# Kernel optimization log

Hardware: AMD Instinct MI355X
Metric: run time of the kernel (lower is better)

The kernel has to match this reference:

```python
import math
import jax, jax.numpy as jnp
import numpy as np

PATCH_NUMS = (1, 2, 3, 4, 5, 6, 8, 10, 13, 16)
_lens = [p * p for p in PATCH_NUMS]
_cum = np.concatenate([[0], np.cumsum(_lens)])
BEGIN_ENDS = [(int(_cum[i]), int(_cum[i + 1])) for i in range(len(PATCH_NUMS))]
L_TOTAL = int(_cum[-1])  # 680

B, C = 32, 1024
S, P, M, R, NCAT = 10, 8, 4, 8, 22
SLOTS = P * M  # 32 slots per scale
MEM_RANK = 64
ALPHA_HID = 128


def setup_inputs() -> dict:
    key = jax.random.key(0)
    ks = jax.random.split(key, 24)
    inp = {}
    inp['x'] = jax.random.normal(ks[0], (B, L_TOTAL, C), jnp.float32)
    # -1 means CFG-unconditional sample (no category memory)
    inp['category_ids'] = jax.random.randint(ks[1], (B,), -1, NCAT)
    # shared memory, orthogonal-ish init rescaled to xavier std sqrt(2/(C+C))
    inp['shared_memory'] = jax.random.normal(ks[2], (S, SLOTS, C)) * math.sqrt(1.0 / C)
    inp['cat_A'] = jax.random.normal(ks[3], (NCAT, S, R)) * 0.01
    inp['cat_B'] = jax.random.normal(ks[4], (S, R, SLOTS * C)) * (1.0 / math.sqrt(R))
    inp['cat_emb'] = jax.random.normal(ks[5], (NCAT, C)) * 0.02
    inp['scale_emb'] = jax.random.normal(ks[6], (S, C)) * 0.02
    inp['Wq'] = jax.random.normal(ks[7], (C, C)) * (1.0 / math.sqrt(C))
    inp['Wk'] = jax.random.normal(ks[8], (C, C)) * (1.0 / math.sqrt(C))
    inp['Wv'] = jax.random.normal(ks[9], (C, C)) * (1.0 / math.sqrt(C))
    inp['aW1'] = jax.random.normal(ks[10], (3 * C, ALPHA_HID)) * (1.0 / math.sqrt(3 * C))
    inp['ab1'] = jnp.zeros((ALPHA_HID,), jnp.float32)
    inp['aW2'] = jax.random.normal(ks[11], (ALPHA_HID, 1)) * 0.01  # init zeros in torch; small random to exercise math
    inp['ab2'] = jnp.full((1,), -1.0, jnp.float32)
    inp['kW1'] = jax.random.normal(ks[12], (C, MEM_RANK)) * (1.0 / math.sqrt(C))
    inp['kb1'] = jnp.zeros((MEM_RANK,), jnp.float32)
    inp['kW2'] = jax.random.normal(ks[13], (MEM_RANK, C)) * (1.0 / math.sqrt(MEM_RANK))
    inp['kb2'] = jnp.zeros((C,), jnp.float32)
    inp['vW1'] = jax.random.normal(ks[14], (C, MEM_RANK)) * (1.0 / math.sqrt(C))
    inp['vb1'] = jnp.zeros((MEM_RANK,), jnp.float32)
    inp['vW2'] = jax.random.normal(ks[15], (MEM_RANK, C)) * (1.0 / math.sqrt(MEM_RANK))
    inp['vb2'] = jnp.zeros((C,), jnp.float32)
    inp['gk_logit'] = jnp.float32(-2.0)  # block_idx=0, depth=16
    inp['gv_logit'] = jnp.float32(-2.0)
    inp['log_temp'] = jnp.float32(math.log(0.1))
    return inp


def reference(x, category_ids, shared_memory, cat_A, cat_B, cat_emb, scale_emb,
              Wq, Wk, Wv, aW1, ab1, aW2, ab2,
              kW1, kb1, kW2, kb2, vW1, vb1, vW2, vb2,
              gk_logit, gv_logit, log_temp):
    Bb, L, Cc = x.shape
    temp = jnp.clip(jnp.exp(log_temp), 0.05, 1.0)
    inv_sqrt_c = 1.0 / math.sqrt(Cc)

    query = x @ Wq                              # [B, L, C]
    shared_k = shared_memory @ Wk               # [S, slots, C]
    shared_v = shared_memory @ Wv

    valid = (category_ids >= 0)                 # [B]
    cid = jnp.clip(category_ids, 0, None)
    a_all = cat_A[cid]                          # [B, S, R]
    ce = cat_emb[cid]                           # [B, C]

    outs = []
    for i, (s, e) in enumerate(BEGIN_ENDS):
        q = query[:, s:e, :]                    # [B, Ls, C]
        Ls = e - s
        V = i + 1                               # visible scales
        # --- shared retrieval over visible slots ---
        ks_ = shared_k[:V].reshape(V * SLOTS, Cc)
        vs_ = shared_v[:V].reshape(V * SLOTS, Cc)
        attn_s = jax.nn.softmax((q @ ks_.T) * inv_sqrt_c / temp, axis=-1)
        o_s = attn_s @ vs_                      # [B, Ls, C]
        # --- per-category memory: shared + low-rank residual ---
        delta = jnp.einsum('bvr,vrd->bvd', a_all[:, :V], cat_B[:V])
        delta = delta.reshape(Bb, V, SLOTS, Cc)
        cat_mem = (shared_memory[:V][None] + delta).reshape(Bb, V * SLOTS, Cc)
        kc = cat_mem @ Wk                       # [B, Vs, C]
        vc = cat_mem @ Wv
        attn_c = jax.nn.softmax(jnp.einsum('bld,bsd->bls', q, kc) * inv_sqrt_c / temp, axis=-1)
        o_c = jnp.einsum('bls,bsd->bld', attn_c, vc)
        # --- learned alpha blend (zeroed for invalid / CFG categories) ---
        ai = jnp.concatenate([
            q,
            jnp.broadcast_to(ce[:, None, :], (Bb, Ls, Cc)),
            jnp.broadcast_to(scale_emb[i][None, None, :], (Bb, Ls, Cc)),
        ], axis=-1)                             # [B, Ls, 3C]
        h = jax.nn.gelu(ai @ aW1 + ab1, approximate=False)
        alpha = jax.nn.sigmoid(h @ aW2 + ab2)   # [B, Ls, 1]
        alpha = jnp.where(valid[:, None, None], alpha, 0.0)
        outs.append(o_s + alpha * (o_c - o_s))

    mem = jnp.concatenate(outs, axis=1)         # [B, L, C]
    mem_k = jax.nn.sigmoid(gk_logit) * ((mem @ kW1 + kb1) @ kW2 + kb2)
    mem_v = jax.nn.sigmoid(gv_logit) * ((mem @ vW1 + vb1) @ vW2 + vb2)
    zero = jnp.float32(0.0)
    return mem_k, mem_v, zero, zero
```

## Files before the change

kernel.cpp:

```cpp
#include <hip/hip_runtime.h>
#include <math.h>

#define NB 32
#define NC 1024
#define LTOT 680

typedef unsigned short u16;
typedef __bf16 bf16x8 __attribute__((ext_vector_type(8)));
typedef float floatx4 __attribute__((ext_vector_type(4)));

__device__ __forceinline__ u16 f2bf(float f)
{
    union { float f; unsigned u; } v; v.f = f;
    unsigned u = v.u;
    u += 0x7FFFu + ((u >> 16) & 1u);
    return (u16)(u >> 16);
}

__device__ __forceinline__ float bf2f(unsigned u)
{
    union { unsigned u; float f; } v; v.u = u << 16; return v.f;
}

__device__ __forceinline__ void gload16(const u16* g, u16* l)
{
    typedef __attribute__((address_space(1))) const void gv_t;
    typedef __attribute__((address_space(3))) void lv_t;
    __builtin_amdgcn_global_load_lds(
        (gv_t*)(unsigned long long)(const void*)g,
        (lv_t*)(unsigned int)(unsigned long long)(void*)l,
        16, 0, 0);
}

__device__ __forceinline__ void slot_decode(int s, int* prow, int* pcq)
{
    *prow = ((s >> 7) << 4) | (s & 15);
    *pcq  = (((s >> 6) & 1) << 2) | ((s >> 4) & 3);
}

template<int AFP32, int OUTBF>
__global__ __launch_bounds__(256) void gemm_mfma(
    const void* __restrict__ Av, const u16* __restrict__ BT,
    float* __restrict__ C, int M, int N, int K, int lda,
    const float* __restrict__ bias, const float* __restrict__ scale_logit)
{
    __shared__ __align__(16) u16 As[16 * 64 * 8];
    __shared__ __align__(16) u16 Bs[16 * 64 * 8];

    const int tid  = threadIdx.x;
    const int m0   = blockIdx.y << 7;
    const int n0   = blockIdx.x << 7;
    const int wave = tid >> 6;
    const int lane = tid & 63;
    const int mh   = wave & 1;
    const int nh   = wave >> 1;

    const u16* aSrc[4];
    const u16* bSrc[4];
#pragma unroll
    for (int p = 0; p < 4; ++p) {
        int s, row, cq;
        s = tid + (p << 8);
        slot_decode(s, &row, &cq);
        if (!AFP32) {
            int gr = m0 + row; if (gr > M - 1) gr = M - 1;
            aSrc[p] = (const u16*)Av + (size_t)gr * lda + (cq << 3);
        }
        int gn = n0 + row; if (gn > N - 1) gn = N - 1;
        bSrc[p] = BT + (size_t)gn * K + (cq << 3);
    }

    floatx4 acc[4][4];
#pragma unroll
    for (int i = 0; i < 4; ++i)
#pragma unroll
        for (int j = 0; j < 4; ++j) acc[i][j] = (floatx4){0.f, 0.f, 0.f, 0.f};

    for (int k0 = 0; k0 < K; k0 += 64) {
        __syncthreads();
        if (AFP32) {
            const float* A = (const float*)Av;
#pragma unroll
            for (int p = 0; p < 8; ++p) {
                int q   = tid + (p << 8);
                int row = q >> 4;
                int fq  = q & 15;
                int gr  = m0 + row; if (gr > M - 1) gr = M - 1;
                const float4 a4 = *(const float4*)(A + (size_t)gr * lda + k0 + (fq << 2));
                int kh = fq >> 3, quad = (fq >> 1) & 3, jh = fq & 1;
                u16* d = &As[((((row >> 4) << 1) | kh) * 64 + (quad << 4) + (row & 15)) * 8 + (jh << 2)];
                d[0] = f2bf(a4.x); d[1] = f2bf(a4.y); d[2] = f2bf(a4.z); d[3] = f2bf(a4.w);
            }
        } else {
#pragma unroll
            for (int p = 0; p < 4; ++p)
                gload16(aSrc[p] + k0, As + ((wave << 6) + (p << 8)) * 8);
        }
#pragma unroll
        for (int p = 0; p < 4; ++p)
            gload16(bSrc[p] + k0, Bs + ((wave << 6) + (p << 8)) * 8);
        __syncthreads();
#pragma unroll
        for (int kh = 0; kh < 2; ++kh) {
            bf16x8 a[4], b[4];
#pragma unroll
            for (int i = 0; i < 4; ++i)
                a[i] = *(const bf16x8*)&As[(((((mh << 2) + i) << 1) | kh) * 64 + lane) * 8];
#pragma unroll
            for (int j = 0; j < 4; ++j)
                b[j] = *(const bf16x8*)&Bs[(((((nh << 2) + j) << 1) | kh) * 64 + lane) * 8];
#pragma unroll
            for (int i = 0; i < 4; ++i)
#pragma unroll
                for (int j = 0; j < 4; ++j)
                    acc[i][j] = __builtin_amdgcn_mfma_f32_16x16x32_bf16(a[i], b[j], acc[i][j], 0, 0, 0);
        }
    }

    float scale = 1.f;
    if (scale_logit) scale = 1.f / (1.f + __expf(-scale_logit[0]));
    const int col = lane & 15, rquad = lane >> 4;
#pragma unroll
    for (int i = 0; i < 4; ++i) {
#pragma unroll
        for (int j = 0; j < 4; ++j) {
#pragma unroll
            for (int r = 0; r < 4; ++r) {
                int gr = m0 + (mh << 6) + (i << 4) + (rquad << 2) + r;
                int gc = n0 + (nh << 6) + (j << 4) + col;
                if (gr < M && gc < N) {
                    float bb = bias ? bias[gc] : 0.f;
                    float val = scale * (acc[i][j][r] + bb);
                    if (OUTBF) ((u16*)C)[(size_t)gr * N + gc] = f2bf(val);
                    else       C[(size_t)gr * N + gc] = val;
                }
            }
        }
    }
}

__global__ __launch_bounds__(256) void gemm_logits(
    const u16* __restrict__ Q, const u16* __restrict__ skb,
    const u16* __restrict__ kcb, float* __restrict__ out)
{
    __shared__ __align__(16) u16 As[16 * 64 * 8];
    __shared__ __align__(16) u16 Bs[16 * 64 * 8];

    const int tid  = threadIdx.x;
    const int m0   = blockIdx.x << 7;
    const int n0   = blockIdx.y << 7;
    const int b    = blockIdx.z;
    const int wave = tid >> 6;
    const int lane = tid & 63;
    const int mh   = wave & 1;
    const int nh   = wave >> 1;

    const u16* Ab = Q   + (size_t)b * 680 * 1024;
    const u16* KC = kcb + (size_t)b * 320 * 1024;

    const u16* aSrc[4];
    const u16* bSrc[4];
#pragma unroll
    for (int p = 0; p < 4; ++p) {
        int s, row, cq;
        s = tid + (p << 8);
        slot_decode(s, &row, &cq);
        int gr = m0 + row; if (gr > 679) gr = 679;
        aSrc[p] = Ab + (size_t)gr * 1024 + (cq << 3);
        int gn = n0 + row;
        bSrc[p] = ((gn < 320) ? (skb + (size_t)gn * 1024)
                              : (KC + (size_t)(gn - 320) * 1024)) + (cq << 3);
    }

    floatx4 acc[4][4];
#pragma unroll
    for (int i = 0; i < 4; ++i)
#pragma unroll
        for (int j = 0; j < 4; ++j) acc[i][j] = (floatx4){0.f, 0.f, 0.f, 0.f};

    for (int k0 = 0; k0 < 1024; k0 += 64) {
        __syncthreads();
#pragma unroll
        for (int p = 0; p < 4; ++p)
            gload16(aSrc[p] + k0, As + ((wave << 6) + (p << 8)) * 8);
#pragma unroll
        for (int p = 0; p < 4; ++p)
            gload16(bSrc[p] + k0, Bs + ((wave << 6) + (p << 8)) * 8);
        __syncthreads();
#pragma unroll
        for (int kh = 0; kh < 2; ++kh) {
            bf16x8 a[4], bb[4];
#pragma unroll
            for (int i = 0; i < 4; ++i)
                a[i] = *(const bf16x8*)&As[(((((mh << 2) + i) << 1) | kh) * 64 + lane) * 8];
#pragma unroll
            for (int j = 0; j < 4; ++j)
                bb[j] = *(const bf16x8*)&Bs[(((((nh << 2) + j) << 1) | kh) * 64 + lane) * 8];
#pragma unroll
            for (int i = 0; i < 4; ++i)
#pragma unroll
                for (int j = 0; j < 4; ++j)
                    acc[i][j] = __builtin_amdgcn_mfma_f32_16x16x32_bf16(a[i], bb[j], acc[i][j], 0, 0, 0);
        }
    }

    const int col = lane & 15, rquad = lane >> 4;
#pragma unroll
    for (int i = 0; i < 4; ++i)
#pragma unroll
        for (int j = 0; j < 4; ++j)
#pragma unroll
            for (int r = 0; r < 4; ++r) {
                int gr = m0 + (mh << 6) + (i << 4) + (rquad << 2) + r;
                int gc = n0 + (nh << 6) + (j << 4) + col;
                if (gr < 680)
                    out[((size_t)b * 680 + gr) * 640 + gc] = acc[i][j][r];
            }
}

__global__ __launch_bounds__(256) void gemm_pv(
    const u16* __restrict__ P, const u16* __restrict__ svT,
    const u16* __restrict__ vcT, u16* __restrict__ out)
{
    __shared__ __align__(16) u16 As[16 * 64 * 8];
    __shared__ __align__(16) u16 Bs[16 * 64 * 8];

    const int tid  = threadIdx.x;
    const int m0   = blockIdx.x << 7;
    const int n0   = blockIdx.y << 7;
    const int b    = blockIdx.z;
    const int wave = tid >> 6;
    const int lane = tid & 63;
    const int mh   = wave & 1;
    const int nh   = wave >> 1;

    const u16* aSrc[4];
    const u16* bSrcS[4];
    const u16* bSrcC[4];
#pragma unroll
    for (int p = 0; p < 4; ++p) {
        int s, row, cq;
        s = tid + (p << 8);
        slot_decode(s, &row, &cq);
        int gr = m0 + row; if (gr > 679) gr = 679;
        aSrc[p] = P + ((size_t)b * 680 + gr) * 1280 + (cq << 3);
        int gn = n0 + row;
        bSrcS[p] = svT + (size_t)gn * 320 + (cq << 3);
        bSrcC[p] = vcT + ((size_t)b * 1024 + gn) * 320 + (cq << 3);
    }

    floatx4 acc[4][4];
#pragma unroll
    for (int i = 0; i < 4; ++i)
#pragma unroll
        for (int j = 0; j < 4; ++j) acc[i][j] = (floatx4){0.f, 0.f, 0.f, 0.f};

    for (int k0 = 0; k0 < 640; k0 += 64) {
        __syncthreads();
#pragma unroll
        for (int p = 0; p < 4; ++p)
            gload16(aSrc[p] + k0, As + ((wave << 6) + (p << 8)) * 8);
#pragma unroll
        for (int p = 0; p < 4; ++p) {
            const u16* bp = (k0 < 320) ? (bSrcS[p] + k0) : (bSrcC[p] + (k0 - 320));
            gload16(bp, Bs + ((wave << 6) + (p << 8)) * 8);
        }
        __syncthreads();
#pragma unroll
        for (int kh = 0; kh < 2; ++kh) {
            bf16x8 a[4], bb[4];
#pragma unroll
            for (int i = 0; i < 4; ++i)
                a[i] = *(const bf16x8*)&As[(((((mh << 2) + i) << 1) | kh) * 64 + lane) * 8];
#pragma unroll
            for (int j = 0; j < 4; ++j)
                bb[j] = *(const bf16x8*)&Bs[(((((nh << 2) + j) << 1) | kh) * 64 + lane) * 8];
#pragma unroll
            for (int i = 0; i < 4; ++i)
#pragma unroll
                for (int j = 0; j < 4; ++j)
                    acc[i][j] = __builtin_amdgcn_mfma_f32_16x16x32_bf16(a[i], bb[j], acc[i][j], 0, 0, 0);
        }
    }

    const int col = lane & 15, rquad = lane >> 4;
#pragma unroll
    for (int i = 0; i < 4; ++i)
#pragma unroll
        for (int j = 0; j < 4; ++j)
#pragma unroll
            for (int r = 0; r < 4; ++r) {
                int gr = m0 + (mh << 6) + (i << 4) + (rquad << 2) + r;
                int gc = n0 + (nh << 6) + (j << 4) + col;
                if (gr < 680)
                    out[((size_t)b * 680 + gr) * 1024 + gc] = f2bf(acc[i][j][r]);
            }
}

__global__ __launch_bounds__(256) void gemm_halpha(
    const u16* __restrict__ Q, const u16* __restrict__ W,
    const float* __restrict__ ceW, const float* __restrict__ seW,
    const int* __restrict__ cat_ids, u16* __restrict__ h)
{
    __shared__ __align__(16) u16 As[16 * 64 * 8];
    __shared__ __align__(16) u16 Bs[16 * 64 * 8];

    const int tid  = threadIdx.x;
    const int m0   = blockIdx.x << 7;
    const int wave = tid >> 6;
    const int lane = tid & 63;
    const int mh   = wave & 1;
    const int nh   = wave >> 1;

    const u16* aSrc[4];
    const u16* bSrc[4];
#pragma unroll
    for (int p = 0; p < 4; ++p) {
        int s, row, cq;
        s = tid + (p << 8);
        slot_decode(s, &row, &cq);
        aSrc[p] = Q + (size_t)(m0 + row) * 1024 + (cq << 3);
        bSrc[p] = W + (size_t)row * 1024 + (cq << 3);
    }

    floatx4 acc[4][4];
#pragma unroll
    for (int i = 0; i < 4; ++i)
#pragma unroll
        for (int j = 0; j < 4; ++j) acc[i][j] = (floatx4){0.f, 0.f, 0.f, 0.f};

    for (int k0 = 0; k0 < 1024; k0 += 64) {
        __syncthreads();
#pragma unroll
        for (int p = 0; p < 4; ++p)
            gload16(aSrc[p] + k0, As + ((wave << 6) + (p << 8)) * 8);
#pragma unroll
        for (int p = 0; p < 4; ++p)
            gload16(bSrc[p] + k0, Bs + ((wave << 6) + (p << 8)) * 8);
        __syncthreads();
#pragma unroll
        for (int kh = 0; kh < 2; ++kh) {
            bf16x8 a[4], bb[4];
#pragma unroll
            for (int i = 0; i < 4; ++i)
                a[i] = *(const bf16x8*)&As[(((((mh << 2) + i) << 1) | kh) * 64 + lane) * 8];
#pragma unroll
            for (int j = 0; j < 4; ++j)
                bb[j] = *(const bf16x8*)&Bs[(((((nh << 2) + j) << 1) | kh) * 64 + lane) * 8];
#pragma unroll
            for (int i = 0; i < 4; ++i)
#pragma unroll
                for (int j = 0; j < 4; ++j)
                    acc[i][j] = __builtin_amdgcn_mfma_f32_16x16x32_bf16(a[i], bb[j], acc[i][j], 0, 0, 0);
        }
    }

    const int se_[9] = {1,5,14,30,55,91,155,255,424};
    const int col = lane & 15, rquad = lane >> 4;
#pragma unroll
    for (int i = 0; i < 4; ++i) {
#pragma unroll
        for (int r = 0; r < 4; ++r) {
            int gr = m0 + (mh << 6) + (i << 4) + (rquad << 2) + r;
            int b  = gr / 680;
            int l  = gr - b * 680;
            int isc = 0;
#pragma unroll
            for (int k = 0; k < 9; ++k) if (l >= se_[k]) isc = k + 1;
            int cid = cat_ids[b]; if (cid < 0) cid = 0;
            const float* cw = ceW + cid * 128;
            const float* sw = seW + isc * 128;
#pragma unroll
            for (int j = 0; j < 4; ++j) {
                int gc = (nh << 6) + (j << 4) + col;
                float val = acc[i][j][r] + cw[gc] + sw[gc];
                float g = 0.5f * val * (1.0f + erff(val * 0.70710678118654752f));
                h[(size_t)gr * 128 + gc] = f2bf(g);
            }
        }
    }
}

__global__ __launch_bounds__(256) void alpha_reduce(
    const u16* __restrict__ h, const float* __restrict__ aW2,
    const float* __restrict__ ab2, const int* __restrict__ cat_ids,
    float* __restrict__ alpha)
{
    const int wave = threadIdx.x >> 6;
    const int lane = threadIdx.x & 63;
    const int row  = (blockIdx.x << 2) + wave;

    const unsigned pk = *(const unsigned*)(h + (size_t)row * 128 + (lane << 1));
    float s = bf2f(pk) * aW2[lane << 1] + bf2f(pk >> 16) * aW2[(lane << 1) + 1];
#pragma unroll
    for (int k = 32; k >= 1; k >>= 1) s += __shfl_xor(s, k);
    if (lane == 0) {
        int b = row / 680;
        float al = 0.f;
        if (cat_ids[b] >= 0) al = 1.f / (1.f + expf(-(s + ab2[0])));
        alpha[row] = al;
    }
}

__global__ __launch_bounds__(256) void softmax_kernel(
    float* __restrict__ logits, const float* __restrict__ alpha,
    const float* __restrict__ log_temp)
{
    const int tid  = threadIdx.x;
    const int w    = tid >> 6;
    const int lane = tid & 63;
    const int b    = blockIdx.y;
    const int l    = (blockIdx.x << 2) + w;

    const int se[10] = {1,5,14,30,55,91,155,255,424,680};
    int isc = 0;
#pragma unroll
    for (int k = 0; k < 9; ++k) if (l >= se[k]) isc = k + 1;
    const int NK = (isc + 1) << 5;

    float temp = __expf(log_temp[0]);
    temp = fminf(fmaxf(temp, 0.05f), 1.0f);
    const float Ksc = 0.03125f / temp;

    float* row = logits + ((size_t)b * 680 + l) * 640;

    float ls[5], lc[5];
#pragma unroll
    for (int u = 0; u < 5; ++u) {
        int j = lane + (u << 6);
        bool v = j < NK;
        ls[u] = v ? row[j]       : -1e30f;
        lc[u] = v ? row[320 + j] : -1e30f;
    }
    float mxs = -1e30f, mxc = -1e30f;
#pragma unroll
    for (int u = 0; u < 5; ++u) { mxs = fmaxf(mxs, ls[u]); mxc = fmaxf(mxc, lc[u]); }
#pragma unroll
    for (int k = 32; k >= 1; k >>= 1) {
        mxs = fmaxf(mxs, __shfl_xor(mxs, k));
        mxc = fmaxf(mxc, __shfl_xor(mxc, k));
    }
    float es[5], ec[5], ss = 0.f, sc = 0.f;
#pragma unroll
    for (int u = 0; u < 5; ++u) {
        int j = lane + (u << 6);
        bool v = j < NK;
        es[u] = v ? __expf((ls[u] - mxs) * Ksc) : 0.f;
        ec[u] = v ? __expf((lc[u] - mxc) * Ksc) : 0.f;
        ss += es[u]; sc += ec[u];
    }
#pragma unroll
    for (int k = 32; k >= 1; k >>= 1) {
        ss += __shfl_xor(ss, k);
        sc += __shfl_xor(sc, k);
    }
    const float al = alpha[b * LTOT + l];
    const float wS = (1.f - al) / ss;
    const float wC = al / sc;

    u16* po = (u16*)row;
#pragma unroll
    for (int u = 0; u < 5; ++u) {
        int j = lane + (u << 6);
        po[j]       = f2bf(es[u] * wS);
        po[320 + j] = f2bf(ec[u] * wC);
    }
}

__global__ __launch_bounds__(256) void castbf(
    const float* __restrict__ in, u16* __restrict__ out, int n4)
{
    int i = blockIdx.x * 256 + threadIdx.x;
    const int stride = gridDim.x * 256;
    for (; i < n4; i += stride) {
        const float4 v = ((const float4*)in)[i];
        uint2 o;
        o.x = (unsigned)f2bf(v.x) | ((unsigned)f2bf(v.y) << 16);
        o.y = (unsigned)f2bf(v.z) | ((unsigned)f2bf(v.w) << 16);
        ((uint2*)out)[i] = o;
    }
}

__global__ __launch_bounds__(256) void tcast(
    const float* __restrict__ in, u16* __restrict__ out, int R, int Cc)
{
    __shared__ float t[32][33];
    const int bx = blockIdx.x * 32;
    const int by = blockIdx.y * 32;
    const int x = threadIdx.x & 31;
    const int y0 = threadIdx.x >> 5;
#pragma unroll
    for (int yy = y0; yy < 32; yy += 8)
        t[yy][x] = (by + yy < R && bx + x < Cc)
                 ? in[(size_t)(by + yy) * Cc + bx + x] : 0.f;
    __syncthreads();
#pragma unroll
    for (int yy = y0; yy < 32; yy += 8)
        if (bx + yy < Cc && by + x < R)
            out[(size_t)(bx + yy) * R + by + x] = f2bf(t[x][yy]);
}

__global__ __launch_bounds__(256) void transpose32(
    const float* __restrict__ in, float* __restrict__ out, int R, int Cc)
{
    __shared__ float t[32][33];
    const int bx = blockIdx.x * 32;
    const int by = blockIdx.y * 32;
    const int x = threadIdx.x & 31;
    const int y0 = threadIdx.x >> 5;
#pragma unroll
    for (int yy = y0; yy < 32; yy += 8)
        t[yy][x] = (by + yy < R && bx + x < Cc)
                 ? in[(size_t)(by + yy) * Cc + bx + x] : 0.f;
    __syncthreads();
#pragma unroll
    for (int yy = y0; yy < 32; yy += 8)
        if (bx + yy < Cc && by + x < R)
            out[(size_t)(bx + yy) * R + by + x] = t[x][yy];
}

__global__ __launch_bounds__(256) void build_kc(
    const float* __restrict__ sk, const float* __restrict__ catBK,
    const float* __restrict__ cat_A, const int* __restrict__ cat_ids,
    u16* __restrict__ kc)
{
    const int b = blockIdx.x;
    const int jrow = blockIdx.y;
    const int v = jrow >> 5, slot = jrow & 31;
    int cid = cat_ids[b]; if (cid < 0) cid = 0;
    float a[8];
#pragma unroll
    for (int r = 0; r < 8; ++r) a[r] = cat_A[(cid * 10 + v) * 8 + r];
    const int c = threadIdx.x << 2;
    float4 acc = *(const float4*)(sk + (size_t)jrow * 1024 + c);
#pragma unroll
    for (int r = 0; r < 8; ++r) {
        const float4 bv = *(const float4*)(catBK + (size_t)((v * 8 + r) * 32 + slot) * 1024 + c);
        acc.x = fmaf(a[r], bv.x, acc.x);
        acc.y = fmaf(a[r], bv.y, acc.y);
        acc.z = fmaf(a[r], bv.z, acc.z);
        acc.w = fmaf(a[r], bv.w, acc.w);
    }
    uint2 pk;
    pk.x = (unsigned)f2bf(acc.x) | ((unsigned)f2bf(acc.y) << 16);
    pk.y = (unsigned)f2bf(acc.z) | ((unsigned)f2bf(acc.w) << 16);
    *(uint2*)(kc + ((size_t)b * 320 + jrow) * 1024 + c) = pk;
}

__global__ __launch_bounds__(320) void build_vcT(
    const float* __restrict__ svT, const float* __restrict__ catBVT,
    const float* __restrict__ cat_A, const int* __restrict__ cat_ids,
    u16* __restrict__ vcT)
{
    __shared__ float aS[80];
    const int b = blockIdx.x;
    const int c = blockIdx.y;
    const int tid = threadIdx.x;
    if (tid < 80) {
        int cid = cat_ids[b]; if (cid < 0) cid = 0;
        aS[tid] = cat_A[cid * 80 + tid];
    }
    __syncthreads();
    const int j = tid;
    const int v = j >> 5, slot = j & 31;
    float acc = svT[(size_t)c * 320 + j];
    const float* row = catBVT + (size_t)c * 2560;
#pragma unroll
    for (int r = 0; r < 8; ++r)
        acc = fmaf(aS[v * 8 + r], row[(v * 8 + r) * 32 + slot], acc);
    vcT[((size_t)b * 1024 + c) * 320 + j] = f2bf(acc);
}

__global__ void concat_bias(const float* __restrict__ a,
                            const float* __restrict__ b, float* __restrict__ o)
{
    int t = threadIdx.x;
    if (t < 64) o[t] = a[t];
    else if (t < 128) o[t] = b[t - 64];
}

__global__ void tail_zero(float* p)
{
    if (threadIdx.x < 2) p[threadIdx.x] = 0.f;
}

extern "C" void kernel_launch(void* const* d_in, const int* in_sizes, int n_in,
                              void* d_out, int out_size, void* d_ws, size_t ws_size,
                              hipStream_t stream)
{
    (void)in_sizes; (void)n_in;
    const float* x         = (const float*)d_in[0];
    const int*   cat_ids   = (const int*)  d_in[1];
    const float* sm        = (const float*)d_in[2];
    const float* cat_A     = (const float*)d_in[3];
    const float* cat_B     = (const float*)d_in[4];
    const float* cat_emb   = (const float*)d_in[5];
    const float* scale_emb = (const float*)d_in[6];
    const float* Wq        = (const float*)d_in[7];
    const float* Wk        = (const float*)d_in[8];
    const float* Wv        = (const float*)d_in[9];
    const float* aW1       = (const float*)d_in[10];
    const float* ab1       = (const float*)d_in[11];
    const float* aW2       = (const float*)d_in[12];
    const float* ab2       = (const float*)d_in[13];
    const float* kW1       = (const float*)d_in[14];
    const float* kb1       = (const float*)d_in[15];
    const float* kW2       = (const float*)d_in[16];
    const float* kb2       = (const float*)d_in[17];
    const float* vW1       = (const float*)d_in[18];
    const float* vb1       = (const float*)d_in[19];
    const float* vW2       = (const float*)d_in[20];
    const float* vb2       = (const float*)d_in[21];
    const float* gk        = (const float*)d_in[22];
    const float* gv        = (const float*)d_in[23];
    const float* log_temp  = (const float*)d_in[24];

    float* out   = (float*)d_out;
    float* memb  = out;
    float* outv  = out + (size_t)21760 * 1024;

    float* w      = (float*)d_ws;
    u16*   kc_bf  = (u16*)w;
    u16*   vcT_bf = (u16*)(w + 5242880);
    float* sk     = w + 10485760;
    float* sv     = w + 10813440;
    float* svT    = w + 11141120;
    u16*   sk_bf  = (u16*)(w + 11468800);
    u16*   svT_bf = (u16*)(w + 11632640);
    float* alph   = w + 11796480;
    float* logits = w + 11859200;
    float* tail0  = w + 25785600;
    u16*   aW1topT = (u16*)tail0;
    u16*   aW1midT = (u16*)(tail0 + 65536);
    u16*   aW1botT = (u16*)(tail0 + 131072);
    float* ceW    = tail0 + 196608;
    float* seW    = tail0 + 199424;
    float* cb     = tail0 + 200704;
    u16*   h_bf   = (u16*)(tail0 + 200832);
    u16*   catB_bf = (u16*)(w + 27379072);
    u16*   sm_bf  = (u16*)(w + 28689792);
    if (ws_size < (size_t)29881600 * 4) return;
    if (out_size < 2 * 21760 * 1024 + 2) return;

    u16*   x_bf   = (u16*)logits;
    float* bufA   = logits + 5570560;
    float* bufB   = bufA + 2621440;
    float* catBVT = bufB + 2621440;
    u16*   WqT    = (u16*)w;
    u16*   WkT    = WqT + 1048576;
    u16*   WvT    = WkT + 1048576;
    u16*   kW1T   = (u16*)sv;
    u16*   vW1T   = kW1T + 65536;
    u16*   kW2T   = vW1T + 65536;
    u16*   vW2T   = kW2T + 65536;
    u16*   bufAB_bf = (u16*)w;
    u16*   mem_bf = (u16*)memb;
    u16*   query_bf = (u16*)outv;

    const dim3 blk256(256);

    castbf<<<dim3(2048), blk256, 0, stream>>>(x, x_bf, 21760 * 1024 / 4);
    castbf<<<dim3(320), blk256, 0, stream>>>(sm, sm_bf, 320 * 1024 / 4);
    castbf<<<dim3(2048), blk256, 0, stream>>>(cat_B, catB_bf, 2560 * 1024 / 4);
    tcast<<<dim3(32, 32), blk256, 0, stream>>>(Wq, WqT, 1024, 1024);
    tcast<<<dim3(32, 32), blk256, 0, stream>>>(Wk, WkT, 1024, 1024);
    tcast<<<dim3(32, 32), blk256, 0, stream>>>(Wv, WvT, 1024, 1024);
    tcast<<<dim3(4, 32), blk256, 0, stream>>>(aW1,              aW1topT, 1024, 128);
    tcast<<<dim3(4, 32), blk256, 0, stream>>>(aW1 + 1024 * 128, aW1midT, 1024, 128);
    tcast<<<dim3(4, 32), blk256, 0, stream>>>(aW1 + 2048 * 128, aW1botT, 1024, 128);

    gemm_mfma<0,1><<<dim3(8, 170), blk256, 0, stream>>>(x_bf,    WqT, (float*)query_bf, 21760, 1024, 1024, 1024, nullptr, nullptr);
    gemm_mfma<0,0><<<dim3(8, 3),   blk256, 0, stream>>>(sm_bf,   WkT, sk,   320,  1024, 1024, 1024, nullptr, nullptr);
    gemm_mfma<0,0><<<dim3(8, 3),   blk256, 0, stream>>>(sm_bf,   WvT, sv,   320,  1024, 1024, 1024, nullptr, nullptr);
    gemm_mfma<0,0><<<dim3(8, 20),  blk256, 0, stream>>>(catB_bf, WkT, bufA, 2560, 1024, 1024, 1024, nullptr, nullptr);
    gemm_mfma<0,0><<<dim3(8, 20),  blk256, 0, stream>>>(catB_bf, WvT, bufB, 2560, 1024, 1024, 1024, nullptr, nullptr);

    gemm_mfma<1,0><<<dim3(1, 1), blk256, 0, stream>>>(cat_emb,   aW1midT, ceW, 22, 128, 1024, 1024, nullptr, nullptr);
    gemm_mfma<1,0><<<dim3(1, 1), blk256, 0, stream>>>(scale_emb, aW1botT, seW, 10, 128, 1024, 1024, ab1, nullptr);

    castbf<<<dim3(320), blk256, 0, stream>>>(sk, sk_bf, 320 * 1024 / 4);
    transpose32<<<dim3(32, 10), blk256, 0, stream>>>(sv, svT, 320, 1024);
    tcast<<<dim3(32, 10), blk256, 0, stream>>>(sv, svT_bf, 320, 1024);
    transpose32<<<dim3(32, 80), blk256, 0, stream>>>(bufB, catBVT, 2560, 1024);
    tcast<<<dim3(2, 32), blk256, 0, stream>>>(kW1, kW1T, 1024, 64);
    tcast<<<dim3(2, 32), blk256, 0, stream>>>(vW1, vW1T, 1024, 64);
    tcast<<<dim3(32, 2), blk256, 0, stream>>>(kW2, kW2T, 64, 1024);
    tcast<<<dim3(32, 2), blk256, 0, stream>>>(vW2, vW2T, 64, 1024);
    concat_bias<<<dim3(1), dim3(128), 0, stream>>>(kb1, vb1, cb);

    build_kc<<<dim3(NB, 320), blk256, 0, stream>>>(sk, bufA, cat_A, cat_ids, kc_bf);
    build_vcT<<<dim3(NB, 1024), dim3(320), 0, stream>>>(svT, catBVT, cat_A, cat_ids, vcT_bf);

    gemm_halpha<<<dim3(170), blk256, 0, stream>>>(query_bf, aW1topT, ceW, seW, cat_ids, h_bf);
    alpha_reduce<<<dim3(5440), blk256, 0, stream>>>(h_bf, aW2, ab2, cat_ids, alph);

    gemm_logits<<<dim3(6, 5, NB), blk256, 0, stream>>>(query_bf, sk_bf, kc_bf, logits);
    softmax_kernel<<<dim3(170, NB), blk256, 0, stream>>>(logits, alph, log_temp);
    gemm_pv<<<dim3(6, 8, NB), blk256, 0, stream>>>((const u16*)logits, svT_bf, vcT_bf, mem_bf);

    gemm_mfma<0,1><<<dim3(1, 170), blk256, 0, stream>>>(mem_bf, kW1T, (float*)bufAB_bf, 21760, 128, 1024, 1024, cb, nullptr);
    gemm_mfma<0,0><<<dim3(8, 170), blk256, 0, stream>>>(bufAB_bf,      kW2T, memb, 21760, 1024, 64, 128, kb2, gk);
    gemm_mfma<0,0><<<dim3(8, 170), blk256, 0, stream>>>(bufAB_bf + 64, vW2T, outv, 21760, 1024, 64, 128, vb2, gv);

    tail_zero<<<1, 64, 0, stream>>>(out + (size_t)2 * 21760 * 1024);
}
```

Baseline: 1.046 ms.

## Double-buffer LDS tiles in all MFMA GEMMs with async prefetch of next k-tile

All four MFMA GEMM kernels now use two LDS buffers. The next k-tile is issued via global_load_lds before computing on the current one, with a vmcnt wait and raw barriers replacing the two __syncthreads per iteration, so global-load latency overlaps the MFMA work. The fp32-A path of gemm_mfma is removed; the small cat_emb and scale_emb inputs are cast to bf16 first and use the bf16 path instead. This doubles LDS use to 64KB per block, which may reduce occupancy.

```diff
diff --git a/kernel.cpp b/kernel.cpp
--- a/kernel.cpp
+++ b/kernel.cpp
@@ -38,14 +38,19 @@
     *pcq  = (((s >> 6) & 1) << 2) | ((s >> 4) & 3);
 }
 
-template<int AFP32, int OUTBF>
+#define WAIT_VM8()  asm volatile("s_waitcnt vmcnt(8)" ::: "memory")
+#define WAIT_VM0()  asm volatile("s_waitcnt vmcnt(0)" ::: "memory")
+#define BAR()       __builtin_amdgcn_s_barrier()
+#define SCHEDB()    __builtin_amdgcn_sched_barrier(0)
+
+template<int OUTBF>
 __global__ __launch_bounds__(256) void gemm_mfma(
-    const void* __restrict__ Av, const u16* __restrict__ BT,
+    const u16* __restrict__ A, const u16* __restrict__ BT,
     float* __restrict__ C, int M, int N, int K, int lda,
     const float* __restrict__ bias, const float* __restrict__ scale_logit)
 {
-    __shared__ __align__(16) u16 As[16 * 64 * 8];
-    __shared__ __align__(16) u16 Bs[16 * 64 * 8];
+    __shared__ __align__(16) u16 As[2][8192];
+    __shared__ __align__(16) u16 Bs[2][8192];
 
     const int tid  = threadIdx.x;
     const int m0   = blockIdx.y << 7;
@@ -54,18 +59,16 @@
     const int lane = tid & 63;
     const int mh   = wave & 1;
     const int nh   = wave >> 1;
+    const int lbase = (wave << 6) * 8;
 
     const u16* aSrc[4];
     const u16* bSrc[4];
 #pragma unroll
     for (int p = 0; p < 4; ++p) {
-        int s, row, cq;
-        s = tid + (p << 8);
+        int s = tid + (p << 8), row, cq;
         slot_decode(s, &row, &cq);
-        if (!AFP32) {
-            int gr = m0 + row; if (gr > M - 1) gr = M - 1;
-            aSrc[p] = (const u16*)Av + (size_t)gr * lda + (cq << 3);
-        }
+        int gr = m0 + row; if (gr > M - 1) gr = M - 1;
+        aSrc[p] = A + (size_t)gr * lda + (cq << 3);
         int gn = n0 + row; if (gn > N - 1) gn = N - 1;
         bSrc[p] = BT + (size_t)gn * K + (cq << 3);
     }
@@ -76,45 +79,41 @@
 #pragma unroll
         for (int j = 0; j < 4; ++j) acc[i][j] = (floatx4){0.f, 0.f, 0.f, 0.f};
 
-    for (int k0 = 0; k0 < K; k0 += 64) {
-        __syncthreads();
-        if (AFP32) {
-            const float* A = (const float*)Av;
-#pragma unroll
-            for (int p = 0; p < 8; ++p) {
-                int q   = tid + (p << 8);
-                int row = q >> 4;
-                int fq  = q & 15;
-                int gr  = m0 + row; if (gr > M - 1) gr = M - 1;
-                const float4 a4 = *(const float4*)(A + (size_t)gr * lda + k0 + (fq << 2));
-                int kh = fq >> 3, quad = (fq >> 1) & 3, jh = fq & 1;
-                u16* d = &As[((((row >> 4) << 1) | kh) * 64 + (quad << 4) + (row & 15)) * 8 + (jh << 2)];
-                d[0] = f2bf(a4.x); d[1] = f2bf(a4.y); d[2] = f2bf(a4.z); d[3] = f2bf(a4.w);
-            }
+#pragma unroll
+    for (int p = 0; p < 4; ++p) gload16(aSrc[p], &As[0][lbase + (p << 11)]);
+#pragma unroll
+    for (int p = 0; p < 4; ++p) gload16(bSrc[p], &Bs[0][lbase + (p << 11)]);
+
+    const int nt = K >> 6;
+    for (int t = 0; t < nt; ++t) {
+        const int cur = t & 1;
+        if (t + 1 < nt) {
+            const int kk = (t + 1) << 6;
+#pragma unroll
+            for (int p = 0; p < 4; ++p) gload16(aSrc[p] + kk, &As[cur ^ 1][lbase + (p << 11)]);
+#pragma unroll
+            for (int p = 0; p < 4; ++p) gload16(bSrc[p] + kk, &Bs[cur ^ 1][lbase + (p << 11)]);
+            WAIT_VM8();
         } else {
-#pragma unroll
-            for (int p = 0; p < 4; ++p)
-                gload16(aSrc[p] + k0, As + ((wave << 6) + (p << 8)) * 8);
-        }
-#pragma unroll
-        for (int p = 0; p < 4; ++p)
-            gload16(bSrc[p] + k0, Bs + ((wave << 6) + (p << 8)) * 8);
-        __syncthreads();
+            WAIT_VM0();
+        }
+        BAR(); SCHEDB();
 #pragma unroll
         for (int kh = 0; kh < 2; ++kh) {
             bf16x8 a[4], b[4];
 #pragma unroll
             for (int i = 0; i < 4; ++i)
-                a[i] = *(const bf16x8*)&As[(((((mh << 2) + i) << 1) | kh) * 64 + lane) * 8];
+                a[i] = *(const bf16x8*)&As[cur][(((((mh << 2) + i) << 1) | kh) * 64 + lane) * 8];
 #pragma unroll
             for (int j = 0; j < 4; ++j)
-                b[j] = *(const bf16x8*)&Bs[(((((nh << 2) + j) << 1) | kh) * 64 + lane) * 8];
+                b[j] = *(const bf16x8*)&Bs[cur][(((((nh << 2) + j) << 1) | kh) * 64 + lane) * 8];
 #pragma unroll
             for (int i = 0; i < 4; ++i)
 #pragma unroll
                 for (int j = 0; j < 4; ++j)
                     acc[i][j] = __builtin_amdgcn_mfma_f32_16x16x32_bf16(a[i], b[j], acc[i][j], 0, 0, 0);
         }
+        SCHEDB(); BAR();
     }
 
     float scale = 1.f;
@@ -143,8 +142,8 @@
     const u16* __restrict__ Q, const u16* __restrict__ skb,
     const u16* __restrict__ kcb, float* __restrict__ out)
 {
-    __shared__ __align__(16) u16 As[16 * 64 * 8];
-    __shared__ __align__(16) u16 Bs[16 * 64 * 8];
+    __shared__ __align__(16) u16 As[2][8192];
+    __shared__ __align__(16) u16 Bs[2][8192];
 
     const int tid  = threadIdx.x;
     const int m0   = blockIdx.x << 7;
@@ -154,6 +153,7 @@
     const int lane = tid & 63;
     const int mh   = wave & 1;
     const int nh   = wave >> 1;
+    const int lbase = (wave << 6) * 8;
 
     const u16* Ab = Q   + (size_t)b * 680 * 1024;
     const u16* KC = kcb + (size_t)b * 320 * 1024;
@@ -162,8 +162,7 @@
     const u16* bSrc[4];
 #pragma unroll
     for (int p = 0; p < 4; ++p) {
-        int s, row, cq;
-        s = tid + (p << 8);
+        int s = tid + (p << 8), row, cq;
         slot_decode(s, &row, &cq);
         int gr = m0 + row; if (gr > 679) gr = 679;
         aSrc[p] = Ab + (size_t)gr * 1024 + (cq << 3);
@@ -178,30 +177,40 @@
 #pragma unroll
         for (int j = 0; j < 4; ++j) acc[i][j] = (floatx4){0.f, 0.f, 0.f, 0.f};
 
-    for (int k0 = 0; k0 < 1024; k0 += 64) {
-        __syncthreads();
-#pragma unroll
-        for (int p = 0; p < 4; ++p)
-            gload16(aSrc[p] + k0, As + ((wave << 6) + (p << 8)) * 8);
-#pragma unroll
-        for (int p = 0; p < 4; ++p)
-            gload16(bSrc[p] + k0, Bs + ((wave << 6) + (p << 8)) * 8);
-        __syncthreads();
+#pragma unroll
+    for (int p = 0; p < 4; ++p) gload16(aSrc[p], &As[0][lbase + (p << 11)]);
+#pragma unroll
+    for (int p = 0; p < 4; ++p) gload16(bSrc[p], &Bs[0][lbase + (p << 11)]);
+
+    for (int t = 0; t < 16; ++t) {
+        const int cur = t & 1;
+        if (t < 15) {
+            const int kk = (t + 1) << 6;
+#pragma unroll
+            for (int p = 0; p < 4; ++p) gload16(aSrc[p] + kk, &As[cur ^ 1][lbase + (p << 11)]);
+#pragma unroll
+            for (int p = 0; p < 4; ++p) gload16(bSrc[p] + kk, &Bs[cur ^ 1][lbase + (p << 11)]);
+            WAIT_VM8();
+        } else {
+            WAIT_VM0();
+        }
+        BAR(); SCHEDB();
 #pragma unroll
         for (int kh = 0; kh < 2; ++kh) {
             bf16x8 a[4], bb[4];
 #pragma unroll
             for (int i = 0; i < 4; ++i)
-                a[i] = *(const bf16x8*)&As[(((((mh << 2) + i) << 1) | kh) * 64 + lane) * 8];
+                a[i] = *(const bf16x8*)&As[cur][(((((mh << 2) + i) << 1) | kh) * 64 + lane) * 8];
 #pragma unroll
             for (int j = 0; j < 4; ++j)
-                bb[j] = *(const bf16x8*)&Bs[(((((nh << 2) + j) << 1) | kh) * 64 + lane) * 8];
+                bb[j] = *(const bf16x8*)&Bs[cur][(((((nh << 2) + j) << 1) | kh) * 64 + lane) * 8];
 #pragma unroll
             for (int i = 0; i < 4; ++i)
 #pragma unroll
                 for (int j = 0; j < 4; ++j)
                     acc[i][j] = __builtin_amdgcn_mfma_f32_16x16x32_bf16(a[i], bb[j], acc[i][j], 0, 0, 0);
         }
+        SCHEDB(); BAR();
     }
 
     const int col = lane & 15, rquad = lane >> 4;
@@ -222,8 +231,8 @@
     const u16* __restrict__ P, const u16* __restrict__ svT,
     const u16* __restrict__ vcT, u16* __restrict__ out)
 {
-    __shared__ __align__(16) u16 As[16 * 64 * 8];
-    __shared__ __align__(16) u16 Bs[16 * 64 * 8];
+    __shared__ __align__(16) u16 As[2][8192];
+    __shared__ __align__(16) u16 Bs[2][8192];
 
     const int tid  = threadIdx.x;
     const int m0   = blockIdx.x << 7;
@@ -233,14 +242,14 @@
     const int lane = tid & 63;
     const int mh   = wave & 1;
     const int nh   = wave >> 1;
+    const int lbase = (wave << 6) * 8;
 
     const u16* aSrc[4];
     const u16* bSrcS[4];
     const u16* bSrcC[4];
 #pragma unroll
     for (int p = 0; p < 4; ++p) {
-        int s, row, cq;
-        s = tid + (p << 8);
+        int s = tid + (p << 8), row, cq;
         slot_decode(s, &row, &cq);
         int gr = m0 + row; if (gr > 679) gr = 679;
         aSrc[p] = P + ((size_t)b * 680 + gr) * 1280 + (cq << 3);
@@ -255,32 +264,44 @@
 #pragma unroll
         for (int j = 0; j < 4; ++j) acc[i][j] = (floatx4){0.f, 0.f, 0.f, 0.f};
 
-    for (int k0 = 0; k0 < 640; k0 += 64) {
-        __syncthreads();
-#pragma unroll
-        for (int p = 0; p < 4; ++p)
-            gload16(aSrc[p] + k0, As + ((wave << 6) + (p << 8)) * 8);
-#pragma unroll
-        for (int p = 0; p < 4; ++p) {
-            const u16* bp = (k0 < 320) ? (bSrcS[p] + k0) : (bSrcC[p] + (k0 - 320));
-            gload16(bp, Bs + ((wave << 6) + (p << 8)) * 8);
-        }
-        __syncthreads();
+#pragma unroll
+    for (int p = 0; p < 4; ++p) gload16(aSrc[p], &As[0][lbase + (p << 11)]);
+#pragma unroll
+    for (int p = 0; p < 4; ++p) gload16(bSrcS[p], &Bs[0][lbase + (p << 11)]);
+
+    for (int t = 0; t < 10; ++t) {
+        const int cur = t & 1;
+        if (t < 9) {
+            const int tn = t + 1;
+            const int kk = tn << 6;
+#pragma unroll
+            for (int p = 0; p < 4; ++p) gload16(aSrc[p] + kk, &As[cur ^ 1][lbase + (p << 11)]);
+#pragma unroll
+            for (int p = 0; p < 4; ++p) {
+                const u16* bp = (tn < 5) ? (bSrcS[p] + kk) : (bSrcC[p] + ((tn - 5) << 6));
+                gload16(bp, &Bs[cur ^ 1][lbase + (p << 11)]);
+            }
+            WAIT_VM8();
+        } else {
+            WAIT_VM0();
+        }
+        BAR(); SCHEDB();
 #pragma unroll
         for (int kh = 0; kh < 2; ++kh) {
             bf16x8 a[4], bb[4];
 #pragma unroll
             for (int i = 0; i < 4; ++i)
-                a[i] = *(const bf16x8*)&As[(((((mh << 2) + i) << 1) | kh) * 64 + lane) * 8];
+                a[i] = *(const bf16x8*)&As[cur][(((((mh << 2) + i) << 1) | kh) * 64 + lane) * 8];
 #pragma unroll
             for (int j = 0; j < 4; ++j)
-                bb[j] = *(const bf16x8*)&Bs[(((((nh << 2) + j) << 1) | kh) * 64 + lane) * 8];
+                bb[j] = *(const bf16x8*)&Bs[cur][(((((nh << 2) + j) << 1) | kh) * 64 + lane) * 8];
 #pragma unroll
             for (int i = 0; i < 4; ++i)
 #pragma unroll
                 for (int j = 0; j < 4; ++j)
                     acc[i][j] = __builtin_amdgcn_mfma_f32_16x16x32_bf16(a[i], bb[j], acc[i][j], 0, 0, 0);
         }
+        SCHEDB(); BAR();
     }
 
     const int col = lane & 15, rquad = lane >> 4;
@@ -302,8 +323,8 @@
     const float* __restrict__ ceW, const float* __restrict__ seW,
     const int* __restrict__ cat_ids, u16* __restrict__ h)
 {
-    __shared__ __align__(16) u16 As[16 * 64 * 8];
-    __shared__ __align__(16) u16 Bs[16 * 64 * 8];
+    __shared__ __align__(16) u16 As[2][8192];
+    __shared__ __align__(16) u16 Bs[2][8192];
 
     const int tid  = threadIdx.x;
     const int m0   = blockIdx.x << 7;
@@ -311,13 +332,13 @@
     const int lane = tid & 63;
     const int mh   = wave & 1;
     const int nh   = wave >> 1;
+    const int lbase = (wave << 6) * 8;
 
     const u16* aSrc[4];
     const u16* bSrc[4];
 #pragma unroll
     for (int p = 0; p < 4; ++p) {
-        int s, row, cq;
-        s = tid + (p << 8);
+        int s = tid + (p << 8), row, cq;
         slot_decode(s, &row, &cq);
         aSrc[p] = Q + (size_t)(m0 + row) * 1024 + (cq << 3);
         bSrc[p] = W + (size_t)row * 1024 + (cq << 3);
@@ -329,30 +350,40 @@
 #pragma unroll
         for (int j = 0; j < 4; ++j) acc[i][j] = (floatx4){0.f, 0.f, 0.f, 0.f};
 
-    for (int k0 = 0; k0 < 1024; k0 += 64) {
-        __syncthreads();
-#pragma unroll
-        for (int p = 0; p < 4; ++p)
-            gload16(aSrc[p] + k0, As + ((wave << 6) + (p << 8)) * 8);
-#pragma unroll
-        for (int p = 0; p < 4; ++p)
-            gload16(bSrc[p] + k0, Bs + ((wave << 6) + (p << 8)) * 8);
-        __syncthreads();
+#pragma unroll
+    for (int p = 0; p < 4; ++p) gload16(aSrc[p], &As[0][lbase + (p << 11)]);
+#pragma unroll
+    for (int p = 0; p < 4; ++p) gload16(bSrc[p], &Bs[0][lbase + (p << 11)]);
+
+    for (int t = 0; t < 16; ++t) {
+        const int cur = t & 1;
+        if (t < 15) {
+            const int kk = (t + 1) << 6;
+#pragma unroll
+            for (int p = 0; p < 4; ++p) gload16(aSrc[p] + kk, &As[cur ^ 1][lbase + (p << 11)]);
+#pragma unroll
+            for (int p = 0; p < 4; ++p) gload16(bSrc[p] + kk, &Bs[cur ^ 1][lbase + (p << 11)]);
+            WAIT_VM8();
+        } else {
+            WAIT_VM0();
+        }
+        BAR(); SCHEDB();
 #pragma unroll
         for (int kh = 0; kh < 2; ++kh) {
             bf16x8 a[4], bb[4];
 #pragma unroll
             for (int i = 0; i < 4; ++i)
-                a[i] = *(const bf16x8*)&As[(((((mh << 2) + i) << 1) | kh) * 64 + lane) * 8];
+                a[i] = *(const bf16x8*)&As[cur][(((((mh << 2) + i) << 1) | kh) * 64 + lane) * 8];
 #pragma unroll
             for (int j = 0; j < 4; ++j)
-                bb[j] = *(const bf16x8*)&Bs[(((((nh << 2) + j) << 1) | kh) * 64 + lane) * 8];
+                bb[j] = *(const bf16x8*)&Bs[cur][(((((nh << 2) + j) << 1) | kh) * 64 + lane) * 8];
 #pragma unroll
             for (int i = 0; i < 4; ++i)
 #pragma unroll
                 for (int j = 0; j < 4; ++j)
                     acc[i][j] = __builtin_amdgcn_mfma_f32_16x16x32_bf16(a[i], bb[j], acc[i][j], 0, 0, 0);
         }
+        SCHEDB(); BAR();
     }
 
     const int se_[9] = {1,5,14,30,55,91,155,255,424};
@@ -639,6 +670,8 @@
     u16*   h_bf   = (u16*)(tail0 + 200832);
     u16*   catB_bf = (u16*)(w + 27379072);
     u16*   sm_bf  = (u16*)(w + 28689792);
+    u16*   ce_bf  = (u16*)(w + 28853632);
+    u16*   se_bf  = (u16*)(w + 28864896);
     if (ws_size < (size_t)29881600 * 4) return;
     if (out_size < 2 * 21760 * 1024 + 2) return;
 
@@ -662,6 +695,8 @@
     castbf<<<dim3(2048), blk256, 0, stream>>>(x, x_bf, 21760 * 1024 / 4);
     castbf<<<dim3(320), blk256, 0, stream>>>(sm, sm_bf, 320 * 1024 / 4);
     castbf<<<dim3(2048), blk256, 0, stream>>>(cat_B, catB_bf, 2560 * 1024 / 4);
+    castbf<<<dim3(22), blk256, 0, stream>>>(cat_emb, ce_bf, 22 * 1024 / 4);
+    castbf<<<dim3(10), blk256, 0, stream>>>(scale_emb, se_bf, 10 * 1024 / 4);
     tcast<<<dim3(32, 32), blk256, 0, stream>>>(Wq, WqT, 1024, 1024);
     tcast<<<dim3(32, 32), blk256, 0, stream>>>(Wk, WkT, 1024, 1024);
     tcast<<<dim3(32, 32), blk256, 0, stream>>>(Wv, WvT, 1024, 1024);
@@ -669,14 +704,14 @@
     tcast<<<dim3(4, 32), blk256, 0, stream>>>(aW1 + 1024 * 128, aW1midT, 1024, 128);
     tcast<<<dim3(4, 32), blk256, 0, stream>>>(aW1 + 2048 * 128, aW1botT, 1024, 128);
 
-    gemm_mfma<0,1><<<dim3(8, 170), blk256, 0, stream>>>(x_bf,    WqT, (float*)query_bf, 21760, 1024, 1024, 1024, nullptr, nullptr);
-    gemm_mfma<0,0><<<dim3(8, 3),   blk256, 0, stream>>>(sm_bf,   WkT, sk,   320,  1024, 1024, 1024, nullptr, nullptr);
-    gemm_mfma<0,0><<<dim3(8, 3),   blk256, 0, stream>>>(sm_bf,   WvT, sv,   320,  1024, 1024, 1024, nullptr, nullptr);
-    gemm_mfma<0,0><<<dim3(8, 20),  blk256, 0, stream>>>(catB_bf, WkT, bufA, 2560, 1024, 1024, 1024, nullptr, nullptr);
-    gemm_mfma<0,0><<<dim3(8, 20),  blk256, 0, stream>>>(catB_bf, WvT, bufB, 2560, 1024, 1024, 1024, nullptr, nullptr);
-
-    gemm_mfma<1,0><<<dim3(1, 1), blk256, 0, stream>>>(cat_emb,   aW1midT, ceW, 22, 128, 1024, 1024, nullptr, nullptr);
-    gemm_mfma<1,0><<<dim3(1, 1), blk256, 0, stream>>>(scale_emb, aW1botT, seW, 10, 128, 1024, 1024, ab1, nullptr);
+    gemm_mfma<1><<<dim3(8, 170), blk256, 0, stream>>>(x_bf,    WqT, (float*)query_bf, 21760, 1024, 1024, 1024, nullptr, nullptr);
+    gemm_mfma<0><<<dim3(8, 3),   blk256, 0, stream>>>(sm_bf,   WkT, sk,   320,  1024, 1024, 1024, nullptr, nullptr);
+    gemm_mfma<0><<<dim3(8, 3),   blk256, 0, stream>>>(sm_bf,   WvT, sv,   320,  1024, 1024, 1024, nullptr, nullptr);
+    gemm_mfma<0><<<dim3(8, 20),  blk256, 0, stream>>>(catB_bf, WkT, bufA, 2560, 1024, 1024, 1024, nullptr, nullptr);
+    gemm_mfma<0><<<dim3(8, 20),  blk256, 0, stream>>>(catB_bf, WvT, bufB, 2560, 1024, 1024, 1024, nullptr, nullptr);
+
+    gemm_mfma<0><<<dim3(1, 1), blk256, 0, stream>>>(ce_bf, aW1midT, ceW, 22, 128, 1024, 1024, nullptr, nullptr);
+    gemm_mfma<0><<<dim3(1, 1), blk256, 0, stream>>>(se_bf, aW1botT, seW, 10, 128, 1024, 1024, ab1, nullptr);
 
     castbf<<<dim3(320), blk256, 0, stream>>>(sk, sk_bf, 320 * 1024 / 4);
     transpose32<<<dim3(32, 10), blk256, 0, stream>>>(sv, svT, 320, 1024);
@@ -698,9 +733,9 @@
     softmax_kernel<<<dim3(170, NB), blk256, 0, stream>>>(logits, alph, log_temp);
     gemm_pv<<<dim3(6, 8, NB), blk256, 0, stream>>>((const u16*)logits, svT_bf, vcT_bf, mem_bf);
 
-    gemm_mfma<0,1><<<dim3(1, 170), blk256, 0, stream>>>(mem_bf, kW1T, (float*)bufAB_bf, 21760, 128, 1024, 1024, cb, nullptr);
-    gemm_mfma<0,0><<<dim3(8, 170), blk256, 0, stream>>>(bufAB_bf,      kW2T, memb, 21760, 1024, 64, 128, kb2, gk);
-    gemm_mfma<0,0><<<dim3(8, 170), blk256, 0, stream>>>(bufAB_bf + 64, vW2T, outv, 21760, 1024, 64, 128, vb2, gv);
+    gemm_mfma<1><<<dim3(1, 170), blk256, 0, stream>>>(mem_bf, kW1T, (float*)bufAB_bf, 21760, 128, 1024, 1024, cb, nullptr);
+    gemm_mfma<0><<<dim3(8, 170), blk256, 0, stream>>>(bufAB_bf,      kW2T, memb, 21760, 1024, 64, 128, kb2, gk);
+    gemm_mfma<0><<<dim3(8, 170), blk256, 0, stream>>>(bufAB_bf + 64, vW2T, outv, 21760, 1024, 64, 128, vb2, gv);
 
     tail_zero<<<1, 64, 0, stream>>>(out + (size_t)2 * 21760 * 1024);
 }
```

Measured after the change: 922.2 us. 11.8% less time.
